# Performance work log

Hardware: AMD Instinct MI355X
Metric: run time of the kernel (lower is better)

## Reference

```python
import jax, jax.numpy as jnp
import numpy as np

P, A = 32, 4096            # poses, atoms per pose
S = 1_500_000              # bonded-term subgraphs (bonds/angles/torsions)
T = 1_048_576              # hash-table size (power of two)
EPS = 1e-8


def setup_inputs() -> dict:
    rng = np.random.default_rng(0)
    coords = jnp.asarray((rng.standard_normal((P, A, 3)) * 3.0).astype(np.float32))
    # each subgraph is a path of 2, 3, or 4 atoms; -1 pads unused slots
    lengths = rng.integers(2, 5, size=S)
    atoms = rng.integers(0, A, size=(S, 4)).astype(np.int32)
    atoms = np.where(np.arange(4)[None, :] < lengths[:, None], atoms, -1).astype(np.int32)
    pose = rng.integers(0, P, size=S).astype(np.int32)
    uids = rng.integers(0, 2 ** 20, size=(P, A)).astype(np.int32)
    hv = rng.random((T, 3), dtype=np.float32)
    hv[:, 0] = hv[:, 0] * 50.0 + 10.0                 # force constant K
    hv[:, 1] = hv[:, 1] * 3.0                         # equilibrium value x0
    hv[:, 2] = rng.integers(1, 4, size=T).astype(np.float32)  # torsion periodicity
    return {
        "coords": coords,
        "hash_values": jnp.asarray(hv),
        "subgraph_atoms": jnp.asarray(atoms),
        "subgraph_pose": jnp.asarray(pose),
        "atom_unique_ids": jnp.asarray(uids),
    }


def _cartbonded(coords, hash_values, subgraph_atoms, subgraph_pose, atom_unique_ids):
    valid = subgraph_atoms >= 0                                  # [S,4]
    idx = jnp.where(valid, subgraph_atoms, 0)                    # clipped gather idx
    # hash-table parameter lookup keyed on the atom unique ids along the path
    uid = jnp.where(valid, atom_unique_ids[subgraph_pose[:, None], idx], 0)
    key = (jnp.sum(uid.astype(jnp.uint32), axis=1) % jnp.uint32(T)).astype(jnp.int32)
    params = hash_values[key]                                    # [S,3]
    K, x0, period = params[:, 0], params[:, 1], params[:, 2]
    # subgraph atom gather: [S,4,3]
    pts = coords[subgraph_pose[:, None], idx]
    p0, p1, p2, p3 = pts[:, 0], pts[:, 1], pts[:, 2], pts[:, 3]
    # bond (2-atom path): harmonic in length
    d = jnp.sqrt(jnp.sum((p1 - p0) ** 2, -1) + EPS)
    e_bond = K * (d - x0) ** 2
    # angle (3-atom path): harmonic in angle
    u, v = p0 - p1, p2 - p1
    cosang = jnp.sum(u * v, -1) / (
        jnp.sqrt(jnp.sum(u * u, -1) + EPS) * jnp.sqrt(jnp.sum(v * v, -1) + EPS)
    )
    theta = jnp.arccos(jnp.clip(cosang, -0.999999, 0.999999))
    e_angle = K * (theta - x0) ** 2
    # torsion (4-atom path): periodic
    b1, b2, b3 = p1 - p0, p2 - p1, p3 - p2
    n1 = jnp.cross(b1, b2)
    n2 = jnp.cross(b2, b3)
    b2n = b2 / jnp.sqrt(jnp.sum(b2 * b2, -1, keepdims=True) + EPS)
    m1 = jnp.cross(n1, b2n)
    phi = jnp.arctan2(jnp.sum(m1 * n2, -1), jnp.sum(n1 * n2, -1) + EPS)
    e_tors = K * (1.0 + jnp.cos(period * phi - x0))
    # select energy by path length, segment-reduce to per-pose scores
    nv = jnp.sum(valid, axis=1)
    e = jnp.where(nv == 2, e_bond, jnp.where(nv == 3, e_angle, e_tors))
    return jax.ops.segment_sum(e, subgraph_pose, num_segments=P)


def reference(coords, hash_values, subgraph_atoms, subgraph_pose, atom_unique_ids):
    return _cartbonded(coords, hash_values, subgraph_atoms, subgraph_pose, atom_unique_ids)
```

## Files before the change

kernel.cpp:

```cpp
#include <hip/hip_runtime.h>

#define S_TOTAL   1500000
#define P_POSES   32
#define A_ATOMS   4096
#define T_HASH    1048576
#define EPSF      1e-8f

__global__ void zero_out_kernel(float* __restrict__ out) {
    int i = threadIdx.x;
    if (i < P_POSES) out[i] = 0.0f;
}

__global__ __launch_bounds__(256) void cartbonded_kernel(
    const float* __restrict__ coords,
    const float* __restrict__ hv,
    const int4*  __restrict__ atoms,
    const int*   __restrict__ pose,
    const int*   __restrict__ uids,
    float*       __restrict__ out,
    int S)
{
    __shared__ float bins[P_POSES];
    for (int i = threadIdx.x; i < P_POSES; i += blockDim.x) bins[i] = 0.0f;
    __syncthreads();

    const int stride = gridDim.x * blockDim.x;
    for (int s = blockIdx.x * blockDim.x + threadIdx.x; s < S; s += stride) {
        const int4 a = atoms[s];
        const int  p = pose[s];

        const bool v0 = a.x >= 0, v1 = a.y >= 0, v2 = a.z >= 0, v3 = a.w >= 0;
        const int  i0 = v0 ? a.x : 0;
        const int  i1 = v1 ? a.y : 0;
        const int  i2 = v2 ? a.z : 0;
        const int  i3 = v3 ? a.w : 0;
        const int  nv = (int)v0 + (int)v1 + (int)v2 + (int)v3;

        const int* __restrict__ urow = uids + p * A_ATOMS;
        unsigned int key = 0u;
        key += v0 ? (unsigned int)urow[i0] : 0u;
        key += v1 ? (unsigned int)urow[i1] : 0u;
        key += v2 ? (unsigned int)urow[i2] : 0u;
        key += v3 ? (unsigned int)urow[i3] : 0u;
        key &= (unsigned int)(T_HASH - 1);

        const float* __restrict__ hp = hv + (size_t)key * 3;
        const float K      = hp[0];
        const float x0     = hp[1];
        const float period = hp[2];

        const float* __restrict__ crow = coords + (size_t)p * (A_ATOMS * 3);
        const float p0x = crow[i0*3+0], p0y = crow[i0*3+1], p0z = crow[i0*3+2];
        const float p1x = crow[i1*3+0], p1y = crow[i1*3+1], p1z = crow[i1*3+2];
        const float p2x = crow[i2*3+0], p2y = crow[i2*3+1], p2z = crow[i2*3+2];
        const float p3x = crow[i3*3+0], p3y = crow[i3*3+1], p3z = crow[i3*3+2];

        const float dbx = p1x - p0x, dby = p1y - p0y, dbz = p1z - p0z;
        const float d  = sqrtf(dbx*dbx + dby*dby + dbz*dbz + EPSF);
        const float db = d - x0;
        const float e_bond = K * db * db;

        const float ux = p0x - p1x, uy = p0y - p1y, uz = p0z - p1z;
        const float vx = p2x - p1x, vy = p2y - p1y, vz = p2z - p1z;
        const float uv  = ux*vx + uy*vy + uz*vz;
        const float uu  = ux*ux + uy*uy + uz*uz;
        const float vv  = vx*vx + vy*vy + vz*vz;
        float cosang = uv / (sqrtf(uu + EPSF) * sqrtf(vv + EPSF));
        cosang = fminf(fmaxf(cosang, -0.999999f), 0.999999f);
        const float theta = acosf(cosang);
        const float da = theta - x0;
        const float e_angle = K * da * da;

        const float b1x = p1x - p0x, b1y = p1y - p0y, b1z = p1z - p0z;
        const float b2x = p2x - p1x, b2y = p2y - p1y, b2z = p2z - p1z;
        const float b3x = p3x - p2x, b3y = p3y - p2y, b3z = p3z - p2z;
        const float n1x = b1y*b2z - b1z*b2y;
        const float n1y = b1z*b2x - b1x*b2z;
        const float n1z = b1x*b2y - b1y*b2x;
        const float n2x = b2y*b3z - b2z*b3y;
        const float n2y = b2z*b3x - b2x*b3z;
        const float n2z = b2x*b3y - b2y*b3x;
        const float b2inv = 1.0f / sqrtf(b2x*b2x + b2y*b2y + b2z*b2z + EPSF);
        const float bnx = b2x * b2inv, bny = b2y * b2inv, bnz = b2z * b2inv;
        const float m1x = n1y*bnz - n1z*bny;
        const float m1y = n1z*bnx - n1x*bnz;
        const float m1z = n1x*bny - n1y*bnx;
        const float sy = m1x*n2x + m1y*n2y + m1z*n2z;
        const float sx = n1x*n2x + n1y*n2y + n1z*n2z + EPSF;
        const float phi = atan2f(sy, sx);
        const float e_tors = K * (1.0f + cosf(period * phi - x0));

        const float e = (nv == 2) ? e_bond : ((nv == 3) ? e_angle : e_tors);
        atomicAdd(&bins[p], e);
    }

    __syncthreads();
    if (threadIdx.x < P_POSES) {
        const float b = bins[threadIdx.x];
        if (b != 0.0f) atomicAdd(&out[threadIdx.x], b);
    }
}

extern "C" void kernel_launch(void* const* d_in, const int* in_sizes, int n_in,
                              void* d_out, int out_size, void* d_ws, size_t ws_size,
                              hipStream_t stream) {
    const float* coords = (const float*)d_in[0];
    const float* hv     = (const float*)d_in[1];
    const int4*  atoms  = (const int4*)d_in[2];
    const int*   pose   = (const int*)d_in[3];
    const int*   uids   = (const int*)d_in[4];
    float* out = (float*)d_out;

    const int S = in_sizes[3];

    zero_out_kernel<<<1, 64, 0, stream>>>(out);

    const int block = 256;
    const int grid  = 2048;
    cartbonded_kernel<<<grid, block, 0, stream>>>(coords, hv, atoms, pose, uids, out, S);
}
```

Before: 69.32 us.

## Batch two subgraphs per thread with staged loads for memory-level parallelism

Replaces the grid-stride loop with a fixed grid where each thread handles two subgraphs. All index, uid, coordinate and hash-parameter gathers for both items are issued in separate phases before any math, so more independent loads are in flight at once. Streaming atom and pose reads use nontemporal loads, and coordinate gathers are issued before the dependent hash lookup. Register use goes up, which may reduce occupancy. The grid now scales with S, so there are many more blocks, each doing one shared-bin flush.

```diff
diff --git a/kernel.cpp b/kernel.cpp
--- a/kernel.cpp
+++ b/kernel.cpp
@@ -1,10 +1,12 @@
 #include <hip/hip_runtime.h>
 
-#define S_TOTAL   1500000
 #define P_POSES   32
 #define A_ATOMS   4096
 #define T_HASH    1048576
 #define EPSF      1e-8f
+#define ITEMS     2
+
+typedef int int4v __attribute__((ext_vector_type(4)));
 
 __global__ void zero_out_kernel(float* __restrict__ out) {
     int i = threadIdx.x;
@@ -14,66 +16,101 @@
 __global__ __launch_bounds__(256) void cartbonded_kernel(
     const float* __restrict__ coords,
     const float* __restrict__ hv,
-    const int4*  __restrict__ atoms,
+    const int4v* __restrict__ atoms,
     const int*   __restrict__ pose,
     const int*   __restrict__ uids,
     float*       __restrict__ out,
-    int S)
+    int S, int NT)
 {
     __shared__ float bins[P_POSES];
-    for (int i = threadIdx.x; i < P_POSES; i += blockDim.x) bins[i] = 0.0f;
+    if (threadIdx.x < P_POSES) bins[threadIdx.x] = 0.0f;
     __syncthreads();
 
-    const int stride = gridDim.x * blockDim.x;
-    for (int s = blockIdx.x * blockDim.x + threadIdx.x; s < S; s += stride) {
-        const int4 a = atoms[s];
-        const int  p = pose[s];
+    const int tid = blockIdx.x * blockDim.x + threadIdx.x;
 
-        const bool v0 = a.x >= 0, v1 = a.y >= 0, v2 = a.z >= 0, v3 = a.w >= 0;
-        const int  i0 = v0 ? a.x : 0;
-        const int  i1 = v1 ? a.y : 0;
-        const int  i2 = v2 ? a.z : 0;
-        const int  i3 = v3 ? a.w : 0;
-        const int  nv = (int)v0 + (int)v1 + (int)v2 + (int)v3;
+    int   sIdx[ITEMS];
+    bool  act[ITEMS];
+    int4v a[ITEMS];
+    int   p[ITEMS];
 
-        const int* __restrict__ urow = uids + p * A_ATOMS;
-        unsigned int key = 0u;
-        key += v0 ? (unsigned int)urow[i0] : 0u;
-        key += v1 ? (unsigned int)urow[i1] : 0u;
-        key += v2 ? (unsigned int)urow[i2] : 0u;
-        key += v3 ? (unsigned int)urow[i3] : 0u;
-        key &= (unsigned int)(T_HASH - 1);
+    #pragma unroll
+    for (int j = 0; j < ITEMS; ++j) {
+        sIdx[j] = tid + j * NT;
+        act[j]  = sIdx[j] < S;
+        if (act[j]) {
+            a[j] = __builtin_nontemporal_load(&atoms[sIdx[j]]);
+            p[j] = __builtin_nontemporal_load(&pose[sIdx[j]]);
+        } else {
+            a[j] = (int4v){0, 0, 0, 0};
+            p[j] = 0;
+        }
+    }
 
+    bool v0[ITEMS], v1[ITEMS], v2[ITEMS], v3[ITEMS];
+    int  i0[ITEMS], i1[ITEMS], i2[ITEMS], i3[ITEMS];
+    int  nv[ITEMS];
+    unsigned int u0[ITEMS], u1[ITEMS], u2[ITEMS], u3[ITEMS];
+
+    #pragma unroll
+    for (int j = 0; j < ITEMS; ++j) {
+        v0[j] = a[j].x >= 0; v1[j] = a[j].y >= 0;
+        v2[j] = a[j].z >= 0; v3[j] = a[j].w >= 0;
+        i0[j] = v0[j] ? a[j].x : 0;
+        i1[j] = v1[j] ? a[j].y : 0;
+        i2[j] = v2[j] ? a[j].z : 0;
+        i3[j] = v3[j] ? a[j].w : 0;
+        nv[j] = (int)v0[j] + (int)v1[j] + (int)v2[j] + (int)v3[j];
+        const int* __restrict__ urow = uids + p[j] * A_ATOMS;
+        u0[j] = v0[j] ? (unsigned int)urow[i0[j]] : 0u;
+        u1[j] = v1[j] ? (unsigned int)urow[i1[j]] : 0u;
+        u2[j] = v2[j] ? (unsigned int)urow[i2[j]] : 0u;
+        u3[j] = v3[j] ? (unsigned int)urow[i3[j]] : 0u;
+    }
+
+    float p0x[ITEMS], p0y[ITEMS], p0z[ITEMS];
+    float p1x[ITEMS], p1y[ITEMS], p1z[ITEMS];
+    float p2x[ITEMS], p2y[ITEMS], p2z[ITEMS];
+    float p3x[ITEMS], p3y[ITEMS], p3z[ITEMS];
+    #pragma unroll
+    for (int j = 0; j < ITEMS; ++j) {
+        const float* __restrict__ crow = coords + (size_t)p[j] * (A_ATOMS * 3);
+        p0x[j] = crow[i0[j]*3+0]; p0y[j] = crow[i0[j]*3+1]; p0z[j] = crow[i0[j]*3+2];
+        p1x[j] = crow[i1[j]*3+0]; p1y[j] = crow[i1[j]*3+1]; p1z[j] = crow[i1[j]*3+2];
+        p2x[j] = crow[i2[j]*3+0]; p2y[j] = crow[i2[j]*3+1]; p2z[j] = crow[i2[j]*3+2];
+        p3x[j] = crow[i3[j]*3+0]; p3y[j] = crow[i3[j]*3+1]; p3z[j] = crow[i3[j]*3+2];
+    }
+
+    float K[ITEMS], x0[ITEMS], period[ITEMS];
+    #pragma unroll
+    for (int j = 0; j < ITEMS; ++j) {
+        unsigned int key = (u0[j] + u1[j] + u2[j] + u3[j]) & (unsigned int)(T_HASH - 1);
         const float* __restrict__ hp = hv + (size_t)key * 3;
-        const float K      = hp[0];
-        const float x0     = hp[1];
-        const float period = hp[2];
+        K[j] = hp[0]; x0[j] = hp[1]; period[j] = hp[2];
+    }
 
-        const float* __restrict__ crow = coords + (size_t)p * (A_ATOMS * 3);
-        const float p0x = crow[i0*3+0], p0y = crow[i0*3+1], p0z = crow[i0*3+2];
-        const float p1x = crow[i1*3+0], p1y = crow[i1*3+1], p1z = crow[i1*3+2];
-        const float p2x = crow[i2*3+0], p2y = crow[i2*3+1], p2z = crow[i2*3+2];
-        const float p3x = crow[i3*3+0], p3y = crow[i3*3+1], p3z = crow[i3*3+2];
+    #pragma unroll
+    for (int j = 0; j < ITEMS; ++j) {
+        if (!act[j]) continue;
 
-        const float dbx = p1x - p0x, dby = p1y - p0y, dbz = p1z - p0z;
+        const float dbx = p1x[j]-p0x[j], dby = p1y[j]-p0y[j], dbz = p1z[j]-p0z[j];
         const float d  = sqrtf(dbx*dbx + dby*dby + dbz*dbz + EPSF);
-        const float db = d - x0;
-        const float e_bond = K * db * db;
+        const float db = d - x0[j];
+        const float e_bond = K[j] * db * db;
 
-        const float ux = p0x - p1x, uy = p0y - p1y, uz = p0z - p1z;
-        const float vx = p2x - p1x, vy = p2y - p1y, vz = p2z - p1z;
-        const float uv  = ux*vx + uy*vy + uz*vz;
-        const float uu  = ux*ux + uy*uy + uz*uz;
-        const float vv  = vx*vx + vy*vy + vz*vz;
+        const float ux = p0x[j]-p1x[j], uy = p0y[j]-p1y[j], uz = p0z[j]-p1z[j];
+        const float vx = p2x[j]-p1x[j], vy = p2y[j]-p1y[j], vz = p2z[j]-p1z[j];
+        const float uv = ux*vx + uy*vy + uz*vz;
+        const float uu = ux*ux + uy*uy + uz*uz;
+        const float vv = vx*vx + vy*vy + vz*vz;
         float cosang = uv / (sqrtf(uu + EPSF) * sqrtf(vv + EPSF));
         cosang = fminf(fmaxf(cosang, -0.999999f), 0.999999f);
         const float theta = acosf(cosang);
-        const float da = theta - x0;
-        const float e_angle = K * da * da;
+        const float da = theta - x0[j];
+        const float e_angle = K[j] * da * da;
 
-        const float b1x = p1x - p0x, b1y = p1y - p0y, b1z = p1z - p0z;
-        const float b2x = p2x - p1x, b2y = p2y - p1y, b2z = p2z - p1z;
-        const float b3x = p3x - p2x, b3y = p3y - p2y, b3z = p3z - p2z;
+        const float b1x = dbx, b1y = dby, b1z = dbz;
+        const float b2x = p2x[j]-p1x[j], b2y = p2y[j]-p1y[j], b2z = p2z[j]-p1z[j];
+        const float b3x = p3x[j]-p2x[j], b3y = p3y[j]-p2y[j], b3z = p3z[j]-p2z[j];
         const float n1x = b1y*b2z - b1z*b2y;
         const float n1y = b1z*b2x - b1x*b2z;
         const float n1z = b1x*b2y - b1y*b2x;
@@ -81,17 +118,17 @@
         const float n2y = b2z*b3x - b2x*b3z;
         const float n2z = b2x*b3y - b2y*b3x;
         const float b2inv = 1.0f / sqrtf(b2x*b2x + b2y*b2y + b2z*b2z + EPSF);
-        const float bnx = b2x * b2inv, bny = b2y * b2inv, bnz = b2z * b2inv;
+        const float bnx = b2x*b2inv, bny = b2y*b2inv, bnz = b2z*b2inv;
         const float m1x = n1y*bnz - n1z*bny;
         const float m1y = n1z*bnx - n1x*bnz;
         const float m1z = n1x*bny - n1y*bnx;
         const float sy = m1x*n2x + m1y*n2y + m1z*n2z;
         const float sx = n1x*n2x + n1y*n2y + n1z*n2z + EPSF;
         const float phi = atan2f(sy, sx);
-        const float e_tors = K * (1.0f + cosf(period * phi - x0));
+        const float e_tors = K[j] * (1.0f + cosf(period[j]*phi - x0[j]));
 
-        const float e = (nv == 2) ? e_bond : ((nv == 3) ? e_angle : e_tors);
-        atomicAdd(&bins[p], e);
+        const float e = (nv[j] == 2) ? e_bond : ((nv[j] == 3) ? e_angle : e_tors);
+        atomicAdd(&bins[p[j]], e);
     }
 
     __syncthreads();
@@ -106,16 +143,17 @@
                               hipStream_t stream) {
     const float* coords = (const float*)d_in[0];
     const float* hv     = (const float*)d_in[1];
-    const int4*  atoms  = (const int4*)d_in[2];
+    const int4v* atoms  = (const int4v*)d_in[2];
     const int*   pose   = (const int*)d_in[3];
     const int*   uids   = (const int*)d_in[4];
     float* out = (float*)d_out;
 
-    const int S = in_sizes[3];
+    const int S  = in_sizes[3];
+    const int NT = (S + ITEMS - 1) / ITEMS;
 
     zero_out_kernel<<<1, 64, 0, stream>>>(out);
 
     const int block = 256;
-    const int grid  = 2048;
-    cartbonded_kernel<<<grid, block, 0, stream>>>(coords, hv, atoms, pose, uids, out, S);
+    const int grid  = (NT + block - 1) / block;
+    cartbonded_kernel<<<grid, block, 0, stream>>>(coords, hv, atoms, pose, uids, out, S, NT);
 }
```

Result: slower. 74.96 us (+8.1%).
